# Performance work log

Measured on AMD Instinct MI355X. Metric: run time of the kernel, lower is better.

Reference implementation:

```python
import jax, jax.numpy as jnp
import numpy as np

N_NODES = 100000
N_EDGES = 3200000
D_IN = 128
D_HID = 128
D_FF = 256
N_CLASSES = 26
N_GRAPHS = 512


def setup_inputs() -> dict:
    key = jax.random.key(0)
    ks = jax.random.split(key, 12)
    s = 0.05
    return {
        "x": jax.random.normal(ks[0], (N_NODES, D_IN), dtype=jnp.float32),
        "edge_index": jax.random.randint(ks[1], (2, N_EDGES), 0, N_NODES, dtype=jnp.int64),
        "batch": jnp.sort(jax.random.randint(ks[2], (N_NODES,), 0, N_GRAPHS, dtype=jnp.int64)),
        "W1": jax.random.normal(ks[3], (D_IN, D_HID), dtype=jnp.float32) * s,
        "b1": jnp.zeros((D_HID,), dtype=jnp.float32),
        "W2": jax.random.normal(ks[4], (D_HID, D_HID), dtype=jnp.float32) * s,
        "b2": jnp.zeros((D_HID,), dtype=jnp.float32),
        "W3": jax.random.normal(ks[5], (D_HID, D_HID), dtype=jnp.float32) * s,
        "b3": jnp.zeros((D_HID,), dtype=jnp.float32),
        "Wfc": jax.random.normal(ks[6], (D_HID, D_FF), dtype=jnp.float32) * s,
        "bfc": jnp.zeros((D_FF,), dtype=jnp.float32),
        "Wfc2": jax.random.normal(ks[7], (D_FF, N_CLASSES), dtype=jnp.float32) * s,
        "bfc2": jnp.zeros((N_CLASSES,), dtype=jnp.float32),
    }


def _gcn_layer(x, src, dst, norm, W, b):
    # GCNConv: h = x @ W; out[dst] += norm_e * h[src]; out += b
    h = x @ W                                   # [N, D]
    msg = h[src] * norm[:, None]                # [E+N, D] gather + scale
    agg = jax.ops.segment_sum(msg, dst, num_segments=N_NODES)
    return agg + b


def reference(x, edge_index, batch, W1, b1, W2, b2, W3, b3, Wfc, bfc, Wfc2, bfc2):
    # add self-loops (PyG GCNConv default) and compute symmetric normalization once
    loop = jnp.arange(N_NODES, dtype=edge_index.dtype)
    src = jnp.concatenate([edge_index[0], loop])
    dst = jnp.concatenate([edge_index[1], loop])
    deg = jax.ops.segment_sum(jnp.ones_like(dst, dtype=x.dtype), dst, num_segments=N_NODES)
    dinv = jnp.where(deg > 0, jax.lax.rsqrt(deg), 0.0)
    norm = dinv[src] * dinv[dst]               # D^{-1/2} A_hat D^{-1/2}

    h = jax.nn.relu(_gcn_layer(x, src, dst, norm, W1, b1))
    h = jax.nn.relu(_gcn_layer(h, src, dst, norm, W2, b2))
    h = jax.nn.relu(_gcn_layer(h, src, dst, norm, W3, b3))

    # global mean pool over graphs
    sums = jax.ops.segment_sum(h, batch, num_segments=N_GRAPHS)       # [G, D]
    cnts = jax.ops.segment_sum(jnp.ones((h.shape[0],), h.dtype), batch, num_segments=N_GRAPHS)
    pooled = sums / jnp.maximum(cnts, 1.0)[:, None]

    out = jax.nn.relu(pooled @ Wfc + bfc)       # dropout is identity at inference
    return out @ Wfc2 + bfc2                    # [G, num_classes]
```

## Files before the change

### kernel.cpp

```cpp
#include <hip/hip_runtime.h>
#include <hip/hip_bf16.h>

typedef __bf16 bf16;
typedef __attribute__((ext_vector_type(8))) __bf16 bf16x8;
typedef __attribute__((ext_vector_type(4))) float f32x4;

constexpr int N_NODES   = 100000;
constexpr int N_PAD     = 100032;
constexpr int D         = 128;
constexpr int D_FF      = 256;
constexpr int N_CLASSES = 26;
constexpr int N_GRAPHS  = 512;
constexpr int NB1       = 256;
constexpr int NBUCK     = (N_NODES + 511) / 512;

__device__ inline float2 bf2f(unsigned u) {
    float lo = __uint_as_float(u << 16);
    float hi = __uint_as_float(u & 0xffff0000u);
    return make_float2(lo, hi);
}

__device__ inline void nt_store_bf16(bf16* p, float f) {
    bf16 v = (bf16)f;
    short s = *reinterpret_cast<short*>(&v);
    __builtin_nontemporal_store(s, reinterpret_cast<short*>(p));
}


__global__ __launch_bounds__(1024) void p1_hist(const int* __restrict__ edst,
                                                int* __restrict__ gcount, int e) {
    __shared__ int cnt[NBUCK];
    for (int t = threadIdx.x; t < NBUCK; t += 1024) cnt[t] = 0;
    __syncthreads();
    int chunk = (e + NB1 - 1) / NB1;
    int lo = blockIdx.x * chunk;
    int hi = min(e, lo + chunk);
    for (int i = lo + threadIdx.x; i < hi; i += 1024)
        atomicAdd(&cnt[edst[i] >> 9], 1);
    __syncthreads();
    for (int t = threadIdx.x; t < NBUCK; t += 1024)
        gcount[t * NB1 + blockIdx.x] = cnt[t];
}

__global__ __launch_bounds__(256) void scan1(const int* __restrict__ in,
                                             int* out, int* bsum, int n) {
    __shared__ int sd[256];
    int i = blockIdx.x * 256 + threadIdx.x;
    int v = (i < n) ? in[i] : 0;
    sd[threadIdx.x] = v; __syncthreads();
    for (int off = 1; off < 256; off <<= 1) {
        int t = (threadIdx.x >= off) ? sd[threadIdx.x - off] : 0;
        __syncthreads();
        sd[threadIdx.x] += t;
        __syncthreads();
    }
    if (i < n) out[i] = sd[threadIdx.x] - v;
    if (threadIdx.x == 255) bsum[blockIdx.x] = sd[255];
}

__global__ __launch_bounds__(1024) void misc_kernel(const int* __restrict__ bsum,
                                                    int* __restrict__ boff, int nb,
                                                    const int* __restrict__ batch,
                                                    int* __restrict__ starts, int n,
                                                    const float* __restrict__ W0,
                                                    const float* __restrict__ W1,
                                                    const float* __restrict__ W2,
                                                    bf16* __restrict__ WT3,
                                                    float* __restrict__ gsum) {
    int t = threadIdx.x;
    if (blockIdx.x == 0) {
        if (t <= N_GRAPHS) {
            int lo = 0, hi = n;
            while (lo < hi) {
                int mid = (lo + hi) >> 1;
                if (batch[mid] < t) lo = mid + 1; else hi = mid;
            }
            starts[t] = lo;
        }
        __shared__ int sd[1024];
        int v = (t < nb) ? bsum[t] : 0;
        sd[t] = v; __syncthreads();
        for (int off = 1; off < 1024; off <<= 1) {
            int x = (t >= off) ? sd[t - off] : 0;
            __syncthreads();
            sd[t] += x;
            __syncthreads();
        }
        if (t < nb) boff[t] = sd[t] - v;
    } else if (blockIdx.x <= 48) {
        int idx = (blockIdx.x - 1) * 1024 + t;
        int l = idx >> 14;
        int rem = idx & 16383;
        int nn = rem >> 7;
        int kk = rem & 127;
        const float* W = (l == 0) ? W0 : (l == 1) ? W1 : W2;
        WT3[idx] = (bf16)W[kk * D + nn];
    } else {
        int idx = (blockIdx.x - 49) * 1024 + t;
        f32x4 z = {0.f, 0.f, 0.f, 0.f};
        *((f32x4*)gsum + idx) = z;
    }
}

__global__ __launch_bounds__(1024) void p3_scatter(const int* __restrict__ esrc,
                                                   const int* __restrict__ edst,
                                                   const int* __restrict__ gbase,
                                                   const int* __restrict__ boff,
                                                   int* __restrict__ ebuf, int e) {
    __shared__ int cur[NBUCK];
    for (int t = threadIdx.x; t < NBUCK; t += 1024)
        cur[t] = gbase[t * NB1 + blockIdx.x] + boff[t];
    __syncthreads();
    int chunk = (e + NB1 - 1) / NB1;
    int lo = blockIdx.x * chunk;
    int hi = min(e, lo + chunk);
    for (int i = lo + threadIdx.x; i < hi; i += 1024) {
        int d = edst[i], s = esrc[i];
        int pos = atomicAdd(&cur[d >> 9], 1);
        ebuf[pos] = (s << 9) | (d & 511);
    }
}

__global__ __launch_bounds__(1024) void p45_fill(const int* __restrict__ ebuf,
                                                 const int* __restrict__ gbase,
                                                 const int* __restrict__ boff,
                                                 float* __restrict__ dinv,
                                                 int* __restrict__ rowptr,
                                                 int* __restrict__ csrc, int e, int n) {
    __shared__ int cnt[512];
    __shared__ int ps[512];
    __shared__ int cur[512];
    int b = blockIdx.x, t = threadIdx.x;
    if (t < 512) cnt[t] = 0;
    __syncthreads();
    int lo = gbase[b * NB1] + boff[b];
    int hi = (b + 1 < NBUCK) ? gbase[(b + 1) * NB1] + boff[b + 1] : e;
    for (int i = lo + t; i < hi; i += 1024)
        atomicAdd(&cnt[ebuf[i] & 511], 1);
    __syncthreads();
    int a = (t < 512) ? cnt[t] : 0;
    if (t < 512) ps[t] = a;
    __syncthreads();
    for (int off = 1; off < 512; off <<= 1) {
        int v = (t >= off && t < 512) ? ps[t - off] : 0;
        __syncthreads();
        if (t < 512) ps[t] += v;
        __syncthreads();
    }
    if (t < 512) {
        int g0 = lo + ps[t] - a;
        int node = b * 512 + t;
        cur[t] = g0;
        if (node < n) {
            rowptr[node] = g0;
            dinv[node] = 1.0f / sqrtf((float)(a + 1));
        }
    }
    if (b == 0 && t == 0) rowptr[n] = e;
    __syncthreads();
    for (int i = lo + t; i < hi; i += 1024) {
        int pe = ebuf[i];
        int pos = atomicAdd(&cur[pe & 511], 1);
        csrc[pos] = pe >> 9;
    }
}


__global__ __launch_bounds__(256) void gemm_f32_kernel(const float* __restrict__ A,
                                                       const bf16* __restrict__ WT,
                                                       bf16* __restrict__ C,
                                                       const float* __restrict__ dinv, int n) {
    int wave = threadIdx.x >> 6;
    int lane = threadIdx.x & 63;
    int m16  = lane & 15;
    int quad = lane >> 4;
    int row0 = blockIdx.x * 64 + wave * 16;
    int arowi = row0 + m16;

    bf16x8 a[4];
    const float* arow = A + (size_t)arowi * D + quad * 8;
#pragma unroll
    for (int kt = 0; kt < 4; ++kt) {
        f32x4 f0 = {0.f, 0.f, 0.f, 0.f};
        f32x4 f1 = {0.f, 0.f, 0.f, 0.f};
        if (arowi < n) {
            f0 = __builtin_nontemporal_load((const f32x4*)(arow + kt * 32));
            f1 = __builtin_nontemporal_load((const f32x4*)(arow + kt * 32 + 4));
        }
        bf16x8 v = { (bf16)f0[0], (bf16)f0[1], (bf16)f0[2], (bf16)f0[3],
                     (bf16)f1[0], (bf16)f1[1], (bf16)f1[2], (bf16)f1[3] };
        a[kt] = v;
    }

    float sc[4];
#pragma unroll
    for (int r = 0; r < 4; ++r) {
        int rr = row0 + quad * 4 + r;
        sc[r] = (rr < n) ? dinv[rr] : 0.f;
    }

#pragma unroll
    for (int nt = 0; nt < 8; ++nt) {
        f32x4 acc = {0.f, 0.f, 0.f, 0.f};
        const bf16* brow = WT + (nt * 16 + m16) * D + quad * 8;
#pragma unroll
        for (int kt = 0; kt < 4; ++kt) {
            bf16x8 b = *(const bf16x8*)(brow + kt * 32);
            acc = __builtin_amdgcn_mfma_f32_16x16x32_bf16(a[kt], b, acc, 0, 0, 0);
        }
#pragma unroll
        for (int r = 0; r < 4; ++r)
            nt_store_bf16(&C[(row0 + quad * 4 + r) * D + nt * 16 + m16], sc[r] * acc[r]);
    }
}

__device__ inline void agg_node(const bf16* __restrict__ h, int v, int n, int c,
                                const int* __restrict__ rowptr,
                                const int* __restrict__ csrc,
                                const float* __restrict__ dinv,
                                float& dv, float acc[8]) {
    int s = 0, e = 0;
    dv = 0.f;
    if (v < n) { s = rowptr[v]; e = rowptr[v + 1]; dv = dinv[v]; }
#pragma unroll
    for (int d = 0; d < 8; ++d) acc[d] = 0.f;
    if (v < n) {
        uint4 u = *(const uint4*)(h + (size_t)v * D + c * 8);
        float2 f0 = bf2f(u.x), f1 = bf2f(u.y), f2 = bf2f(u.z), f3 = bf2f(u.w);
        acc[0] = f0.x; acc[1] = f0.y; acc[2] = f1.x; acc[3] = f1.y;
        acc[4] = f2.x; acc[5] = f2.y; acc[6] = f3.x; acc[7] = f3.y;
    }
    int j = s;
    for (; j + 3 < e; j += 4) {
        int s0 = __builtin_nontemporal_load(csrc + j);
        int s1 = __builtin_nontemporal_load(csrc + j + 1);
        int s2 = __builtin_nontemporal_load(csrc + j + 2);
        int s3 = __builtin_nontemporal_load(csrc + j + 3);
        uint4 u0 = *(const uint4*)(h + (size_t)s0 * D + c * 8);
        uint4 u1 = *(const uint4*)(h + (size_t)s1 * D + c * 8);
        uint4 u2 = *(const uint4*)(h + (size_t)s2 * D + c * 8);
        uint4 u3 = *(const uint4*)(h + (size_t)s3 * D + c * 8);
        {
            float2 a0 = bf2f(u0.x), a1 = bf2f(u0.y), a2 = bf2f(u0.z), a3 = bf2f(u0.w);
            acc[0] += a0.x; acc[1] += a0.y; acc[2] += a1.x; acc[3] += a1.y;
            acc[4] += a2.x; acc[5] += a2.y; acc[6] += a3.x; acc[7] += a3.y;
        }
        {
            float2 a0 = bf2f(u1.x), a1 = bf2f(u1.y), a2 = bf2f(u1.z), a3 = bf2f(u1.w);
            acc[0] += a0.x; acc[1] += a0.y; acc[2] += a1.x; acc[3] += a1.y;
            acc[4] += a2.x; acc[5] += a2.y; acc[6] += a3.x; acc[7] += a3.y;
        }
        {
            float2 a0 = bf2f(u2.x), a1 = bf2f(u2.y), a2 = bf2f(u2.z), a3 = bf2f(u2.w);
            acc[0] += a0.x; acc[1] += a0.y; acc[2] += a1.x; acc[3] += a1.y;
            acc[4] += a2.x; acc[5] += a2.y; acc[6] += a3.x; acc[7] += a3.y;
        }
        {
            float2 a0 = bf2f(u3.x), a1 = bf2f(u3.y), a2 = bf2f(u3.z), a3 = bf2f(u3.w);
            acc[0] += a0.x; acc[1] += a0.y; acc[2] += a1.x; acc[3] += a1.y;
            acc[4] += a2.x; acc[5] += a2.y; acc[6] += a3.x; acc[7] += a3.y;
        }
    }
    for (; j < e; ++j) {
        int s0 = __builtin_nontemporal_load(csrc + j);
        uint4 u0 = *(const uint4*)(h + (size_t)s0 * D + c * 8);
        float2 a0 = bf2f(u0.x), a1 = bf2f(u0.y), a2 = bf2f(u0.z), a3 = bf2f(u0.w);
        acc[0] += a0.x; acc[1] += a0.y; acc[2] += a1.x; acc[3] += a1.y;
        acc[4] += a2.x; acc[5] += a2.y; acc[6] += a3.x; acc[7] += a3.y;
    }
}

__global__ __launch_bounds__(256) void spmm_gemm_kernel(const bf16* __restrict__ h,
                                                        const int* __restrict__ rowptr,
                                                        const int* __restrict__ csrc,
                                                        const float* __restrict__ dinv,
                                                        const float* __restrict__ bias,
                                                        const bf16* __restrict__ WT,
                                                        bf16* __restrict__ C, int n) {
    __shared__ bf16 tile[16][136];
    int t = threadIdx.x;
    int grp = t >> 4;
    int c   = t & 15;
    int v   = blockIdx.x * 16 + grp;
    float dv, acc[8];
    agg_node(h, v, n, c, rowptr, csrc, dinv, dv, acc);
    {
        float4 bi0 = *(const float4*)(bias + c * 8);
        float4 bi1 = *(const float4*)(bias + c * 8 + 4);
        bf16x8 o;
        o[0] = (bf16)fmaxf(fmaf(dv, acc[0], bi0.x), 0.f);
        o[1] = (bf16)fmaxf(fmaf(dv, acc[1], bi0.y), 0.f);
        o[2] = (bf16)fmaxf(fmaf(dv, acc[2], bi0.z), 0.f);
        o[3] = (bf16)fmaxf(fmaf(dv, acc[3], bi0.w), 0.f);
        o[4] = (bf16)fmaxf(fmaf(dv, acc[4], bi1.x), 0.f);
        o[5] = (bf16)fmaxf(fmaf(dv, acc[5], bi1.y), 0.f);
        o[6] = (bf16)fmaxf(fmaf(dv, acc[6], bi1.z), 0.f);
        o[7] = (bf16)fmaxf(fmaf(dv, acc[7], bi1.w), 0.f);
        *(bf16x8*)(&tile[grp][c * 8]) = o;
    }
    __syncthreads();

    int wave = t >> 6, lane = t & 63;
    int m16 = lane & 15, quad = lane >> 4;
    bf16x8 a[4];
#pragma unroll
    for (int kt = 0; kt < 4; ++kt)
        a[kt] = *(const bf16x8*)(&tile[m16][quad * 8 + kt * 32]);

    int base = blockIdx.x * 16;
    float sc[4];
#pragma unroll
    for (int r = 0; r < 4; ++r) {
        int rr = base + quad * 4 + r;
        sc[r] = (rr < n) ? dinv[rr] : 0.f;
    }

#pragma unroll
    for (int nt2 = 0; nt2 < 2; ++nt2) {
        int nt = wave * 2 + nt2;
        f32x4 accq = {0.f, 0.f, 0.f, 0.f};
        const bf16* brow = WT + (nt * 16 + m16) * D + quad * 8;
#pragma unroll
        for (int kt = 0; kt < 4; ++kt) {
            bf16x8 b = *(const bf16x8*)(brow + kt * 32);
            accq = __builtin_amdgcn_mfma_f32_16x16x32_bf16(a[kt], b, accq, 0, 0, 0);
        }
#pragma unroll
        for (int r = 0; r < 4; ++r)
            nt_store_bf16(&C[(size_t)(base + quad * 4 + r) * D + nt * 16 + m16],
                          sc[r] * accq[r]);
    }
}

__global__ __launch_bounds__(256) void spmm2_pool_kernel(const bf16* __restrict__ h,
                                                         const int* __restrict__ rowptr,
                                                         const int* __restrict__ csrc,
                                                         const float* __restrict__ dinv,
                                                         const float* __restrict__ bias,
                                                         const int* __restrict__ batch,
                                                         float* __restrict__ gsum, int n) {
    __shared__ float tile[16][D];
    __shared__ int gid[16];
    int t = threadIdx.x;
    int grp = t >> 4;
    int c   = t & 15;
    int v   = blockIdx.x * 16 + grp;
    float dv, acc[8];
    agg_node(h, v, n, c, rowptr, csrc, dinv, dv, acc);
    float4 bi0 = *(const float4*)(bias + c * 8);
    float4 bi1 = *(const float4*)(bias + c * 8 + 4);
    float r0 = fmaxf(fmaf(dv, acc[0], bi0.x), 0.f);
    float r1 = fmaxf(fmaf(dv, acc[1], bi0.y), 0.f);
    float r2 = fmaxf(fmaf(dv, acc[2], bi0.z), 0.f);
    float r3 = fmaxf(fmaf(dv, acc[3], bi0.w), 0.f);
    float r4 = fmaxf(fmaf(dv, acc[4], bi1.x), 0.f);
    float r5 = fmaxf(fmaf(dv, acc[5], bi1.y), 0.f);
    float r6 = fmaxf(fmaf(dv, acc[6], bi1.z), 0.f);
    float r7 = fmaxf(fmaf(dv, acc[7], bi1.w), 0.f);
    if (v >= n) { r0 = r1 = r2 = r3 = r4 = r5 = r6 = r7 = 0.f; }
    tile[grp][c * 8 + 0] = r0; tile[grp][c * 8 + 1] = r1;
    tile[grp][c * 8 + 2] = r2; tile[grp][c * 8 + 3] = r3;
    tile[grp][c * 8 + 4] = r4; tile[grp][c * 8 + 5] = r5;
    tile[grp][c * 8 + 6] = r6; tile[grp][c * 8 + 7] = r7;
    if (c == 0) gid[grp] = (v < n) ? batch[v] : -1;
    __syncthreads();
    if (t < D) {
        int curg = gid[0];
        float sum = 0.f;
        if (curg >= 0) {
#pragma unroll 1
            for (int k = 0; k < 16; ++k) {
                int gg = gid[k];
                if (gg < 0) break;
                if (gg != curg) {
                    atomicAdd(&gsum[(size_t)curg * D + t], sum);
                    curg = gg; sum = 0.f;
                }
                sum += tile[k][t];
            }
            atomicAdd(&gsum[(size_t)curg * D + t], sum);
        }
    }
}

__global__ __launch_bounds__(256) void fc_head_kernel(const float* __restrict__ gsum,
                                                      const int* __restrict__ starts,
                                                      const float* __restrict__ Wfc,
                                                      const float* __restrict__ bfc,
                                                      const float* __restrict__ Wfc2,
                                                      const float* __restrict__ bfc2,
                                                      float* __restrict__ out) {
    __shared__ float pr[D];
    __shared__ float hid[D_FF];
    __shared__ float red[N_CLASSES][9];
    int g = blockIdx.x, t = threadIdx.x;
    if (t < D) {
        float ccount = fmaxf((float)(starts[g + 1] - starts[g]), 1.0f);
        pr[t] = gsum[(size_t)g * D + t] / ccount;
    }
    __syncthreads();
    float a0 = 0.f, a1 = 0.f, a2 = 0.f, a3 = 0.f;
    for (int k = 0; k < D; k += 4) {
        a0 = fmaf(pr[k],     Wfc[k * D_FF + t],       a0);
        a1 = fmaf(pr[k + 1], Wfc[(k + 1) * D_FF + t], a1);
        a2 = fmaf(pr[k + 2], Wfc[(k + 2) * D_FF + t], a2);
        a3 = fmaf(pr[k + 3], Wfc[(k + 3) * D_FF + t], a3);
    }
    hid[t] = fmaxf((a0 + a1) + (a2 + a3) + bfc[t], 0.f);
    __syncthreads();
    if (t < N_CLASSES * 8) {
        int cls = t >> 3, kk = t & 7;
        float o = 0.f;
        for (int k = kk; k < D_FF; k += 8)
            o = fmaf(hid[k], Wfc2[k * N_CLASSES + cls], o);
        red[cls][kk] = o;
    }
    __syncthreads();
    if (t < N_CLASSES) {
        float o = bfc2[t];
#pragma unroll
        for (int k = 0; k < 8; ++k) o += red[t][k];
        out[g * N_CLASSES + t] = o;
    }
}


extern "C" void kernel_launch(void* const* d_in, const int* in_sizes, int n_in,
                              void* d_out, int out_size, void* d_ws, size_t ws_size,
                              hipStream_t stream) {
    const float* x     = (const float*)d_in[0];
    const int*   eidx  = (const int*)d_in[1];
    const int*   batch = (const int*)d_in[2];
    const float* W[3]  = { (const float*)d_in[3], (const float*)d_in[5], (const float*)d_in[7] };
    const float* b[3]  = { (const float*)d_in[4], (const float*)d_in[6], (const float*)d_in[8] };
    const float* Wfc   = (const float*)d_in[9];
    const float* bfc   = (const float*)d_in[10];
    const float* Wfc2  = (const float*)d_in[11];
    const float* bfc2  = (const float*)d_in[12];
    float* out = (float*)d_out;

    const int E = in_sizes[1] / 2;
    const int N = in_sizes[0] / D;
    const int* esrc = eidx;
    const int* edst = eidx + E;

    uint8_t* base = (uint8_t*)d_ws;
    size_t off = 0;
    auto alloc = [&](size_t bytes) -> void* {
        void* p = base + off;
        off = (off + bytes + 255) & ~(size_t)255;
        return p;
    };
    bf16*  hA     = (bf16*) alloc((size_t)N_PAD * D * 2);
    bf16*  hB     = (bf16*) alloc((size_t)N_PAD * D * 2);
    bf16*  WT3    = (bf16*) alloc((size_t)3 * D * D * 2);
    int*   csrc   = (int*)  alloc((size_t)E * 4);
    int*   ebuf   = (int*)  alloc((size_t)E * 4);
    int*   gcount = (int*)  alloc((size_t)NBUCK * NB1 * 4);
    int*   gbase  = (int*)  alloc((size_t)(NBUCK * NB1 + 1) * 4);
    int*   rowptr = (int*)  alloc((size_t)(N + 1) * 4);
    float* dinv   = (float*)alloc((size_t)N * 4);
    int*   bsum   = (int*)  alloc(4096);
    int*   boff   = (int*)  alloc(4096);
    int*   starts = (int*)  alloc((size_t)(N_GRAPHS + 1) * 4);
    float* gsum   = (float*)alloc((size_t)N_GRAPHS * D * 4);
    (void)ws_size; (void)n_in; (void)out_size;

    const int GB  = N_PAD / 64;
    const int SGB = (N + 15) / 16;
    const int GCN = NBUCK * NB1;
    const int GCB = (GCN + 255) / 256;

    p1_hist<<<NB1, 1024, 0, stream>>>(edst, gcount, E);
    scan1<<<GCB, 256, 0, stream>>>(gcount, gbase, bsum, GCN);
    misc_kernel<<<65, 1024, 0, stream>>>(bsum, boff, GCB, batch, starts, N,
                                         W[0], W[1], W[2], WT3, gsum);
    p3_scatter<<<NB1, 1024, 0, stream>>>(esrc, edst, gbase, boff, ebuf, E);
    p45_fill<<<NBUCK, 1024, 0, stream>>>(ebuf, gbase, boff, dinv, rowptr, csrc, E, N);

    gemm_f32_kernel<<<GB, 256, 0, stream>>>(x, WT3, hA, dinv, N);
    spmm_gemm_kernel<<<SGB, 256, 0, stream>>>(hA, rowptr, csrc, dinv, b[0],
                                              WT3 + (size_t)1 * D * D, hB, N);
    spmm_gemm_kernel<<<SGB, 256, 0, stream>>>(hB, rowptr, csrc, dinv, b[1],
                                              WT3 + (size_t)2 * D * D, hA, N);
    spmm2_pool_kernel<<<SGB, 256, 0, stream>>>(hA, rowptr, csrc, dinv, b[2],
                                               batch, gsum, N);

    fc_head_kernel<<<N_GRAPHS, 256, 0, stream>>>(gsum, starts, Wfc, bfc, Wfc2, bfc2, out);
}
```

Baseline: 617.6 us.

## Pre-sort edges by source bucket before CSR build; drop nontemporal loads/stores

Adds an extra bucket pass keyed on source node, so edges are grouped by source before the destination bucket scatter. Within each destination row the neighbor indices then come out roughly ordered by source, which should improve cache locality of the feature gathers in the SpMM kernels. It also replaces the nontemporal loads and stores with plain ones, so data can stay in cache. The cost is an extra histogram, scan and scatter over all 3.2M edges plus two extra edge arrays.

```diff
diff --git a/kernel.cpp b/kernel.cpp
--- a/kernel.cpp
+++ b/kernel.cpp
@@ -20,14 +20,8 @@
     return make_float2(lo, hi);
 }
 
-__device__ inline void nt_store_bf16(bf16* p, float f) {
-    bf16 v = (bf16)f;
-    short s = *reinterpret_cast<short*>(&v);
-    __builtin_nontemporal_store(s, reinterpret_cast<short*>(p));
-}
-
-
-__global__ __launch_bounds__(1024) void p1_hist(const int* __restrict__ edst,
+
+__global__ __launch_bounds__(1024) void p1_hist(const int* __restrict__ key,
                                                 int* __restrict__ gcount, int e) {
     __shared__ int cnt[NBUCK];
     for (int t = threadIdx.x; t < NBUCK; t += 1024) cnt[t] = 0;
@@ -36,7 +30,7 @@
     int lo = blockIdx.x * chunk;
     int hi = min(e, lo + chunk);
     for (int i = lo + threadIdx.x; i < hi; i += 1024)
-        atomicAdd(&cnt[edst[i] >> 9], 1);
+        atomicAdd(&cnt[key[i] >> 9], 1);
     __syncthreads();
     for (int t = threadIdx.x; t < NBUCK; t += 1024)
         gcount[t * NB1 + blockIdx.x] = cnt[t];
@@ -58,9 +52,22 @@
     if (threadIdx.x == 255) bsum[blockIdx.x] = sd[255];
 }
 
-__global__ __launch_bounds__(1024) void misc_kernel(const int* __restrict__ bsum,
-                                                    int* __restrict__ boff, int nb,
-                                                    const int* __restrict__ batch,
+__global__ __launch_bounds__(1024) void scan2k(const int* __restrict__ bsum,
+                                               int* __restrict__ boff, int nb) {
+    __shared__ int sd[1024];
+    int t = threadIdx.x;
+    int v = (t < nb) ? bsum[t] : 0;
+    sd[t] = v; __syncthreads();
+    for (int off = 1; off < 1024; off <<= 1) {
+        int x = (t >= off) ? sd[t - off] : 0;
+        __syncthreads();
+        sd[t] += x;
+        __syncthreads();
+    }
+    if (t < nb) boff[t] = sd[t] - v;
+}
+
+__global__ __launch_bounds__(1024) void misc_kernel(const int* __restrict__ batch,
                                                     int* __restrict__ starts, int n,
                                                     const float* __restrict__ W0,
                                                     const float* __restrict__ W1,
@@ -77,16 +84,6 @@
             }
             starts[t] = lo;
         }
-        __shared__ int sd[1024];
-        int v = (t < nb) ? bsum[t] : 0;
-        sd[t] = v; __syncthreads();
-        for (int off = 1; off < 1024; off <<= 1) {
-            int x = (t >= off) ? sd[t - off] : 0;
-            __syncthreads();
-            sd[t] += x;
-            __syncthreads();
-        }
-        if (t < nb) boff[t] = sd[t] - v;
     } else if (blockIdx.x <= 48) {
         int idx = (blockIdx.x - 1) * 1024 + t;
         int l = idx >> 14;
@@ -102,8 +99,28 @@
     }
 }
 
-__global__ __launch_bounds__(1024) void p3_scatter(const int* __restrict__ esrc,
-                                                   const int* __restrict__ edst,
+__global__ __launch_bounds__(1024) void p3s_scatter(const int* __restrict__ esrc,
+                                                    const int* __restrict__ edst,
+                                                    const int* __restrict__ gbaseS,
+                                                    const int* __restrict__ boffS,
+                                                    int* __restrict__ esrc2,
+                                                    int* __restrict__ edst2, int e) {
+    __shared__ int cur[NBUCK];
+    for (int t = threadIdx.x; t < NBUCK; t += 1024)
+        cur[t] = gbaseS[t * NB1 + blockIdx.x] + boffS[t];
+    __syncthreads();
+    int chunk = (e + NB1 - 1) / NB1;
+    int lo = blockIdx.x * chunk;
+    int hi = min(e, lo + chunk);
+    for (int i = lo + threadIdx.x; i < hi; i += 1024) {
+        int s = esrc[i], d = edst[i];
+        int pos = atomicAdd(&cur[s >> 9], 1);
+        esrc2[pos] = s; edst2[pos] = d;
+    }
+}
+
+__global__ __launch_bounds__(1024) void p3_scatter(const int* __restrict__ esrc2,
+                                                   const int* __restrict__ edst2,
                                                    const int* __restrict__ gbase,
                                                    const int* __restrict__ boff,
                                                    int* __restrict__ ebuf, int e) {
@@ -115,7 +132,7 @@
     int lo = blockIdx.x * chunk;
     int hi = min(e, lo + chunk);
     for (int i = lo + threadIdx.x; i < hi; i += 1024) {
-        int d = edst[i], s = esrc[i];
+        int d = edst2[i], s = esrc2[i];
         int pos = atomicAdd(&cur[d >> 9], 1);
         ebuf[pos] = (s << 9) | (d & 511);
     }
@@ -181,14 +198,14 @@
     const float* arow = A + (size_t)arowi * D + quad * 8;
 #pragma unroll
     for (int kt = 0; kt < 4; ++kt) {
-        f32x4 f0 = {0.f, 0.f, 0.f, 0.f};
-        f32x4 f1 = {0.f, 0.f, 0.f, 0.f};
+        float4 f0 = make_float4(0.f, 0.f, 0.f, 0.f);
+        float4 f1 = make_float4(0.f, 0.f, 0.f, 0.f);
         if (arowi < n) {
-            f0 = __builtin_nontemporal_load((const f32x4*)(arow + kt * 32));
-            f1 = __builtin_nontemporal_load((const f32x4*)(arow + kt * 32 + 4));
-        }
-        bf16x8 v = { (bf16)f0[0], (bf16)f0[1], (bf16)f0[2], (bf16)f0[3],
-                     (bf16)f1[0], (bf16)f1[1], (bf16)f1[2], (bf16)f1[3] };
+            f0 = *(const float4*)(arow + kt * 32);
+            f1 = *(const float4*)(arow + kt * 32 + 4);
+        }
+        bf16x8 v = { (bf16)f0.x, (bf16)f0.y, (bf16)f0.z, (bf16)f0.w,
+                     (bf16)f1.x, (bf16)f1.y, (bf16)f1.z, (bf16)f1.w };
         a[kt] = v;
     }
 
@@ -210,7 +227,7 @@
         }
 #pragma unroll
         for (int r = 0; r < 4; ++r)
-            nt_store_bf16(&C[(row0 + quad * 4 + r) * D + nt * 16 + m16], sc[r] * acc[r]);
+            C[(row0 + quad * 4 + r) * D + nt * 16 + m16] = (bf16)(sc[r] * acc[r]);
     }
 }
 
@@ -232,10 +249,7 @@
     }
     int j = s;
     for (; j + 3 < e; j += 4) {
-        int s0 = __builtin_nontemporal_load(csrc + j);
-        int s1 = __builtin_nontemporal_load(csrc + j + 1);
-        int s2 = __builtin_nontemporal_load(csrc + j + 2);
-        int s3 = __builtin_nontemporal_load(csrc + j + 3);
+        int s0 = csrc[j], s1 = csrc[j + 1], s2 = csrc[j + 2], s3 = csrc[j + 3];
         uint4 u0 = *(const uint4*)(h + (size_t)s0 * D + c * 8);
         uint4 u1 = *(const uint4*)(h + (size_t)s1 * D + c * 8);
         uint4 u2 = *(const uint4*)(h + (size_t)s2 * D + c * 8);
@@ -262,7 +276,7 @@
         }
     }
     for (; j < e; ++j) {
-        int s0 = __builtin_nontemporal_load(csrc + j);
+        int s0 = csrc[j];
         uint4 u0 = *(const uint4*)(h + (size_t)s0 * D + c * 8);
         float2 a0 = bf2f(u0.x), a1 = bf2f(u0.y), a2 = bf2f(u0.z), a3 = bf2f(u0.w);
         acc[0] += a0.x; acc[1] += a0.y; acc[2] += a1.x; acc[3] += a1.y;
@@ -327,8 +341,7 @@
         }
 #pragma unroll
         for (int r = 0; r < 4; ++r)
-            nt_store_bf16(&C[(size_t)(base + quad * 4 + r) * D + nt * 16 + m16],
-                          sc[r] * accq[r]);
+            C[(size_t)(base + quad * 4 + r) * D + nt * 16 + m16] = (bf16)(sc[r] * accq[r]);
     }
 }
 
@@ -451,19 +464,25 @@
         off = (off + bytes + 255) & ~(size_t)255;
         return p;
     };
-    bf16*  hA     = (bf16*) alloc((size_t)N_PAD * D * 2);
-    bf16*  hB     = (bf16*) alloc((size_t)N_PAD * D * 2);
-    bf16*  WT3    = (bf16*) alloc((size_t)3 * D * D * 2);
-    int*   csrc   = (int*)  alloc((size_t)E * 4);
-    int*   ebuf   = (int*)  alloc((size_t)E * 4);
-    int*   gcount = (int*)  alloc((size_t)NBUCK * NB1 * 4);
-    int*   gbase  = (int*)  alloc((size_t)(NBUCK * NB1 + 1) * 4);
-    int*   rowptr = (int*)  alloc((size_t)(N + 1) * 4);
-    float* dinv   = (float*)alloc((size_t)N * 4);
-    int*   bsum   = (int*)  alloc(4096);
-    int*   boff   = (int*)  alloc(4096);
-    int*   starts = (int*)  alloc((size_t)(N_GRAPHS + 1) * 4);
-    float* gsum   = (float*)alloc((size_t)N_GRAPHS * D * 4);
+    bf16*  hA      = (bf16*) alloc((size_t)N_PAD * D * 2);
+    bf16*  hB      = (bf16*) alloc((size_t)N_PAD * D * 2);
+    bf16*  WT3     = (bf16*) alloc((size_t)3 * D * D * 2);
+    int*   csrc    = (int*)  alloc((size_t)E * 4);
+    int*   ebuf    = (int*)  alloc((size_t)E * 4);
+    int*   esrc2   = (int*)  alloc((size_t)E * 4);
+    int*   edst2   = (int*)  alloc((size_t)E * 4);
+    int*   gcountS = (int*)  alloc((size_t)NBUCK * NB1 * 4);
+    int*   gbaseS  = (int*)  alloc((size_t)(NBUCK * NB1 + 1) * 4);
+    int*   gcountD = (int*)  alloc((size_t)NBUCK * NB1 * 4);
+    int*   gbaseD  = (int*)  alloc((size_t)(NBUCK * NB1 + 1) * 4);
+    int*   rowptr  = (int*)  alloc((size_t)(N + 1) * 4);
+    float* dinv    = (float*)alloc((size_t)N * 4);
+    int*   bsumS   = (int*)  alloc(4096);
+    int*   boffS   = (int*)  alloc(4096);
+    int*   bsumD   = (int*)  alloc(4096);
+    int*   boffD   = (int*)  alloc(4096);
+    int*   starts  = (int*)  alloc((size_t)(N_GRAPHS + 1) * 4);
+    float* gsum    = (float*)alloc((size_t)N_GRAPHS * D * 4);
     (void)ws_size; (void)n_in; (void)out_size;
 
     const int GB  = N_PAD / 64;
@@ -471,12 +490,16 @@
     const int GCN = NBUCK * NB1;
     const int GCB = (GCN + 255) / 256;
 
-    p1_hist<<<NB1, 1024, 0, stream>>>(edst, gcount, E);
-    scan1<<<GCB, 256, 0, stream>>>(gcount, gbase, bsum, GCN);
-    misc_kernel<<<65, 1024, 0, stream>>>(bsum, boff, GCB, batch, starts, N,
-                                         W[0], W[1], W[2], WT3, gsum);
-    p3_scatter<<<NB1, 1024, 0, stream>>>(esrc, edst, gbase, boff, ebuf, E);
-    p45_fill<<<NBUCK, 1024, 0, stream>>>(ebuf, gbase, boff, dinv, rowptr, csrc, E, N);
+    p1_hist<<<NB1, 1024, 0, stream>>>(esrc, gcountS, E);
+    scan1<<<GCB, 256, 0, stream>>>(gcountS, gbaseS, bsumS, GCN);
+    scan2k<<<1, 1024, 0, stream>>>(bsumS, boffS, GCB);
+    misc_kernel<<<65, 1024, 0, stream>>>(batch, starts, N, W[0], W[1], W[2], WT3, gsum);
+    p3s_scatter<<<NB1, 1024, 0, stream>>>(esrc, edst, gbaseS, boffS, esrc2, edst2, E);
+    p1_hist<<<NB1, 1024, 0, stream>>>(edst2, gcountD, E);
+    scan1<<<GCB, 256, 0, stream>>>(gcountD, gbaseD, bsumD, GCN);
+    scan2k<<<1, 1024, 0, stream>>>(bsumD, boffD, GCB);
+    p3_scatter<<<NB1, 1024, 0, stream>>>(esrc2, edst2, gbaseD, boffD, ebuf, E);
+    p45_fill<<<NBUCK, 1024, 0, stream>>>(ebuf, gbaseD, boffD, dinv, rowptr, csrc, E, N);
 
     gemm_f32_kernel<<<GB, 256, 0, stream>>>(x, WT3, hA, dinv, N);
     spmm_gemm_kernel<<<SGB, 256, 0, stream>>>(hA, rowptr, csrc, dinv, b[0],
```

Result: no change. 606.1 us (-1.9%).

## Phase-partition CSR by source range and process node batches per block in lockstep

Applied to the files above, without the earlier changes.

Edges of each destination are now sorted into 13 source-range phases (src>>13), with per-node phase offsets stored in a new P array instead of rowptr. The SpMM kernels use 512 persistent blocks, each covering 196 nodes. They walk all nodes' edges phase by phase so concurrent gathers hit a narrow source window and stay cache-resident, then run the GEMM/pool epilogue in 32-row chunks. This adds extra shared-memory counting in the fill, more registers (7x8 accumulators) and serialized per-chunk syncs. It also moves the boff scan into its own kernel and drops nontemporal loads and stores.

```diff
diff --git a/kernel.cpp b/kernel.cpp
--- a/kernel.cpp
+++ b/kernel.cpp
@@ -14,16 +14,21 @@
 constexpr int NB1       = 256;
 constexpr int NBUCK     = (N_NODES + 511) / 512;
 
+constexpr int KPH  = 13;
+constexpr int PST  = 14;
+constexpr int NPB  = 196;
+constexpr int PBLK = 512;
+
 __device__ inline float2 bf2f(unsigned u) {
     float lo = __uint_as_float(u << 16);
     float hi = __uint_as_float(u & 0xffff0000u);
     return make_float2(lo, hi);
 }
 
-__device__ inline void nt_store_bf16(bf16* p, float f) {
-    bf16 v = (bf16)f;
-    short s = *reinterpret_cast<short*>(&v);
-    __builtin_nontemporal_store(s, reinterpret_cast<short*>(p));
+__device__ inline void acc_row(float acc[8], uint4 u) {
+    float2 f0 = bf2f(u.x), f1 = bf2f(u.y), f2 = bf2f(u.z), f3 = bf2f(u.w);
+    acc[0] += f0.x; acc[1] += f0.y; acc[2] += f1.x; acc[3] += f1.y;
+    acc[4] += f2.x; acc[5] += f2.y; acc[6] += f3.x; acc[7] += f3.y;
 }
 
 
@@ -58,9 +63,22 @@
     if (threadIdx.x == 255) bsum[blockIdx.x] = sd[255];
 }
 
-__global__ __launch_bounds__(1024) void misc_kernel(const int* __restrict__ bsum,
-                                                    int* __restrict__ boff, int nb,
-                                                    const int* __restrict__ batch,
+__global__ __launch_bounds__(1024) void scan2k(const int* __restrict__ bsum,
+                                               int* __restrict__ boff, int nb) {
+    __shared__ int sd[1024];
+    int t = threadIdx.x;
+    int v = (t < nb) ? bsum[t] : 0;
+    sd[t] = v; __syncthreads();
+    for (int off = 1; off < 1024; off <<= 1) {
+        int x = (t >= off) ? sd[t - off] : 0;
+        __syncthreads();
+        sd[t] += x;
+        __syncthreads();
+    }
+    if (t < nb) boff[t] = sd[t] - v;
+}
+
+__global__ __launch_bounds__(1024) void misc_kernel(const int* __restrict__ batch,
                                                     int* __restrict__ starts, int n,
                                                     const float* __restrict__ W0,
                                                     const float* __restrict__ W1,
@@ -77,16 +95,6 @@
             }
             starts[t] = lo;
         }
-        __shared__ int sd[1024];
-        int v = (t < nb) ? bsum[t] : 0;
-        sd[t] = v; __syncthreads();
-        for (int off = 1; off < 1024; off <<= 1) {
-            int x = (t >= off) ? sd[t - off] : 0;
-            __syncthreads();
-            sd[t] += x;
-            __syncthreads();
-        }
-        if (t < nb) boff[t] = sd[t] - v;
     } else if (blockIdx.x <= 48) {
         int idx = (blockIdx.x - 1) * 1024 + t;
         int l = idx >> 14;
@@ -125,21 +133,29 @@
                                                  const int* __restrict__ gbase,
                                                  const int* __restrict__ boff,
                                                  float* __restrict__ dinv,
-                                                 int* __restrict__ rowptr,
+                                                 int* __restrict__ P,
                                                  int* __restrict__ csrc, int e, int n) {
-    __shared__ int cnt[512];
+    __shared__ int c2[512 * KPH];
     __shared__ int ps[512];
-    __shared__ int cur[512];
     int b = blockIdx.x, t = threadIdx.x;
-    if (t < 512) cnt[t] = 0;
+    for (int q = t; q < 512 * KPH; q += 1024) c2[q] = 0;
     __syncthreads();
     int lo = gbase[b * NB1] + boff[b];
     int hi = (b + 1 < NBUCK) ? gbase[(b + 1) * NB1] + boff[b + 1] : e;
-    for (int i = lo + t; i < hi; i += 1024)
-        atomicAdd(&cnt[ebuf[i] & 511], 1);
-    __syncthreads();
-    int a = (t < 512) ? cnt[t] : 0;
-    if (t < 512) ps[t] = a;
+    for (int i = lo + t; i < hi; i += 1024) {
+        int pe = ebuf[i];
+        atomicAdd(&c2[(pe & 511) * KPH + (pe >> 22)], 1);
+    }
+    __syncthreads();
+    int tot = 0;
+    if (t < 512) {
+        for (int k = 0; k < KPH; ++k) {
+            int cc = c2[t * KPH + k];
+            c2[t * KPH + k] = tot;
+            tot += cc;
+        }
+        ps[t] = tot;
+    }
     __syncthreads();
     for (int off = 1; off < 512; off <<= 1) {
         int v = (t >= off && t < 512) ? ps[t - off] : 0;
@@ -148,19 +164,22 @@
         __syncthreads();
     }
     if (t < 512) {
-        int g0 = lo + ps[t] - a;
+        int g0 = lo + ps[t] - tot;
         int node = b * 512 + t;
-        cur[t] = g0;
         if (node < n) {
-            rowptr[node] = g0;
-            dinv[node] = 1.0f / sqrtf((float)(a + 1));
-        }
-    }
-    if (b == 0 && t == 0) rowptr[n] = e;
+            dinv[node] = 1.0f / sqrtf((float)(tot + 1));
+            for (int k = 0; k < KPH; ++k) {
+                int a = g0 + c2[t * KPH + k];
+                P[node * PST + k] = a;
+                c2[t * KPH + k] = a;
+            }
+            P[node * PST + KPH] = g0 + tot;
+        }
+    }
     __syncthreads();
     for (int i = lo + t; i < hi; i += 1024) {
         int pe = ebuf[i];
-        int pos = atomicAdd(&cur[pe & 511], 1);
+        int pos = atomicAdd(&c2[(pe & 511) * KPH + (pe >> 22)], 1);
         csrc[pos] = pe >> 9;
     }
 }
@@ -181,14 +200,14 @@
     const float* arow = A + (size_t)arowi * D + quad * 8;
 #pragma unroll
     for (int kt = 0; kt < 4; ++kt) {
-        f32x4 f0 = {0.f, 0.f, 0.f, 0.f};
-        f32x4 f1 = {0.f, 0.f, 0.f, 0.f};
+        float4 f0 = make_float4(0.f, 0.f, 0.f, 0.f);
+        float4 f1 = make_float4(0.f, 0.f, 0.f, 0.f);
         if (arowi < n) {
-            f0 = __builtin_nontemporal_load((const f32x4*)(arow + kt * 32));
-            f1 = __builtin_nontemporal_load((const f32x4*)(arow + kt * 32 + 4));
-        }
-        bf16x8 v = { (bf16)f0[0], (bf16)f0[1], (bf16)f0[2], (bf16)f0[3],
-                     (bf16)f1[0], (bf16)f1[1], (bf16)f1[2], (bf16)f1[3] };
+            f0 = *(const float4*)(arow + kt * 32);
+            f1 = *(const float4*)(arow + kt * 32 + 4);
+        }
+        bf16x8 v = { (bf16)f0.x, (bf16)f0.y, (bf16)f0.z, (bf16)f0.w,
+                     (bf16)f1.x, (bf16)f1.y, (bf16)f1.z, (bf16)f1.w };
         a[kt] = v;
     }
 
@@ -210,175 +229,171 @@
         }
 #pragma unroll
         for (int r = 0; r < 4; ++r)
-            nt_store_bf16(&C[(row0 + quad * 4 + r) * D + nt * 16 + m16], sc[r] * acc[r]);
-    }
-}
-
-__device__ inline void agg_node(const bf16* __restrict__ h, int v, int n, int c,
-                                const int* __restrict__ rowptr,
-                                const int* __restrict__ csrc,
-                                const float* __restrict__ dinv,
-                                float& dv, float acc[8]) {
-    int s = 0, e = 0;
-    dv = 0.f;
-    if (v < n) { s = rowptr[v]; e = rowptr[v + 1]; dv = dinv[v]; }
-#pragma unroll
-    for (int d = 0; d < 8; ++d) acc[d] = 0.f;
-    if (v < n) {
-        uint4 u = *(const uint4*)(h + (size_t)v * D + c * 8);
-        float2 f0 = bf2f(u.x), f1 = bf2f(u.y), f2 = bf2f(u.z), f3 = bf2f(u.w);
-        acc[0] = f0.x; acc[1] = f0.y; acc[2] = f1.x; acc[3] = f1.y;
-        acc[4] = f2.x; acc[5] = f2.y; acc[6] = f3.x; acc[7] = f3.y;
-    }
-    int j = s;
-    for (; j + 3 < e; j += 4) {
-        int s0 = __builtin_nontemporal_load(csrc + j);
-        int s1 = __builtin_nontemporal_load(csrc + j + 1);
-        int s2 = __builtin_nontemporal_load(csrc + j + 2);
-        int s3 = __builtin_nontemporal_load(csrc + j + 3);
-        uint4 u0 = *(const uint4*)(h + (size_t)s0 * D + c * 8);
-        uint4 u1 = *(const uint4*)(h + (size_t)s1 * D + c * 8);
-        uint4 u2 = *(const uint4*)(h + (size_t)s2 * D + c * 8);
-        uint4 u3 = *(const uint4*)(h + (size_t)s3 * D + c * 8);
-        {
-            float2 a0 = bf2f(u0.x), a1 = bf2f(u0.y), a2 = bf2f(u0.z), a3 = bf2f(u0.w);
-            acc[0] += a0.x; acc[1] += a0.y; acc[2] += a1.x; acc[3] += a1.y;
-            acc[4] += a2.x; acc[5] += a2.y; acc[6] += a3.x; acc[7] += a3.y;
-        }
-        {
-            float2 a0 = bf2f(u1.x), a1 = bf2f(u1.y), a2 = bf2f(u1.z), a3 = bf2f(u1.w);
-            acc[0] += a0.x; acc[1] += a0.y; acc[2] += a1.x; acc[3] += a1.y;
-            acc[4] += a2.x; acc[5] += a2.y; acc[6] += a3.x; acc[7] += a3.y;
-        }
-        {
-            float2 a0 = bf2f(u2.x), a1 = bf2f(u2.y), a2 = bf2f(u2.z), a3 = bf2f(u2.w);
-            acc[0] += a0.x; acc[1] += a0.y; acc[2] += a1.x; acc[3] += a1.y;
-            acc[4] += a2.x; acc[5] += a2.y; acc[6] += a3.x; acc[7] += a3.y;
-        }
-        {
-            float2 a0 = bf2f(u3.x), a1 = bf2f(u3.y), a2 = bf2f(u3.z), a3 = bf2f(u3.w);
-            acc[0] += a0.x; acc[1] += a0.y; acc[2] += a1.x; acc[3] += a1.y;
-            acc[4] += a2.x; acc[5] += a2.y; acc[6] += a3.x; acc[7] += a3.y;
-        }
-    }
-    for (; j < e; ++j) {
-        int s0 = __builtin_nontemporal_load(csrc + j);
-        uint4 u0 = *(const uint4*)(h + (size_t)s0 * D + c * 8);
-        float2 a0 = bf2f(u0.x), a1 = bf2f(u0.y), a2 = bf2f(u0.z), a3 = bf2f(u0.w);
-        acc[0] += a0.x; acc[1] += a0.y; acc[2] += a1.x; acc[3] += a1.y;
-        acc[4] += a2.x; acc[5] += a2.y; acc[6] += a3.x; acc[7] += a3.y;
-    }
-}
-
-__global__ __launch_bounds__(256) void spmm_gemm_kernel(const bf16* __restrict__ h,
-                                                        const int* __restrict__ rowptr,
-                                                        const int* __restrict__ csrc,
-                                                        const float* __restrict__ dinv,
-                                                        const float* __restrict__ bias,
-                                                        const bf16* __restrict__ WT,
-                                                        bf16* __restrict__ C, int n) {
-    __shared__ bf16 tile[16][136];
+            C[(row0 + quad * 4 + r) * D + nt * 16 + m16] = (bf16)(sc[r] * acc[r]);
+    }
+}
+
+__device__ inline void pagg(const bf16* __restrict__ h,
+                            const int* __restrict__ P,
+                            const int* __restrict__ csrc,
+                            int base, int g, int c, int n, float acc[7][8]) {
+#pragma unroll
+    for (int i = 0; i < 7; ++i) {
+#pragma unroll
+        for (int d = 0; d < 8; ++d) acc[i][d] = 0.f;
+        int v = base + i * 32 + g;
+        if (i * 32 + g < NPB && v < n) {
+            uint4 u = *(const uint4*)(h + (size_t)v * D + c * 8);
+            acc_row(acc[i], u);
+        }
+    }
+    for (int k = 0; k < KPH; ++k) {
+#pragma unroll
+        for (int i = 0; i < 7; ++i) {
+            int v = base + i * 32 + g;
+            if (i * 32 + g >= NPB || v >= n) continue;
+            int s = P[v * PST + k], e = P[v * PST + k + 1];
+            int j = s;
+            for (; j + 1 < e; j += 2) {
+                int s0 = csrc[j], s1 = csrc[j + 1];
+                uint4 u0 = *(const uint4*)(h + (size_t)s0 * D + c * 8);
+                uint4 u1 = *(const uint4*)(h + (size_t)s1 * D + c * 8);
+                acc_row(acc[i], u0);
+                acc_row(acc[i], u1);
+            }
+            if (j < e) {
+                int s0 = csrc[j];
+                uint4 u0 = *(const uint4*)(h + (size_t)s0 * D + c * 8);
+                acc_row(acc[i], u0);
+            }
+        }
+    }
+}
+
+__global__ __launch_bounds__(512, 4) void pspmm_gemm_kernel(const bf16* __restrict__ h,
+                                                            const int* __restrict__ P,
+                                                            const int* __restrict__ csrc,
+                                                            const float* __restrict__ dinv,
+                                                            const float* __restrict__ bias,
+                                                            const bf16* __restrict__ WT,
+                                                            bf16* __restrict__ C, int n) {
+    __shared__ bf16 tile[32][136];
     int t = threadIdx.x;
-    int grp = t >> 4;
-    int c   = t & 15;
-    int v   = blockIdx.x * 16 + grp;
-    float dv, acc[8];
-    agg_node(h, v, n, c, rowptr, csrc, dinv, dv, acc);
-    {
-        float4 bi0 = *(const float4*)(bias + c * 8);
-        float4 bi1 = *(const float4*)(bias + c * 8 + 4);
-        bf16x8 o;
-        o[0] = (bf16)fmaxf(fmaf(dv, acc[0], bi0.x), 0.f);
-        o[1] = (bf16)fmaxf(fmaf(dv, acc[1], bi0.y), 0.f);
-        o[2] = (bf16)fmaxf(fmaf(dv, acc[2], bi0.z), 0.f);
-        o[3] = (bf16)fmaxf(fmaf(dv, acc[3], bi0.w), 0.f);
-        o[4] = (bf16)fmaxf(fmaf(dv, acc[4], bi1.x), 0.f);
-        o[5] = (bf16)fmaxf(fmaf(dv, acc[5], bi1.y), 0.f);
-        o[6] = (bf16)fmaxf(fmaf(dv, acc[6], bi1.z), 0.f);
-        o[7] = (bf16)fmaxf(fmaf(dv, acc[7], bi1.w), 0.f);
-        *(bf16x8*)(&tile[grp][c * 8]) = o;
-    }
-    __syncthreads();
+    int g = t >> 4, c = t & 15;
+    int base = blockIdx.x * NPB;
+    float acc[7][8];
+    pagg(h, P, csrc, base, g, c, n, acc);
 
     int wave = t >> 6, lane = t & 63;
     int m16 = lane & 15, quad = lane >> 4;
-    bf16x8 a[4];
-#pragma unroll
-    for (int kt = 0; kt < 4; ++kt)
-        a[kt] = *(const bf16x8*)(&tile[m16][quad * 8 + kt * 32]);
-
-    int base = blockIdx.x * 16;
-    float sc[4];
-#pragma unroll
-    for (int r = 0; r < 4; ++r) {
-        int rr = base + quad * 4 + r;
-        sc[r] = (rr < n) ? dinv[rr] : 0.f;
-    }
-
-#pragma unroll
-    for (int nt2 = 0; nt2 < 2; ++nt2) {
-        int nt = wave * 2 + nt2;
-        f32x4 accq = {0.f, 0.f, 0.f, 0.f};
-        const bf16* brow = WT + (nt * 16 + m16) * D + quad * 8;
-#pragma unroll
-        for (int kt = 0; kt < 4; ++kt) {
-            bf16x8 b = *(const bf16x8*)(brow + kt * 32);
-            accq = __builtin_amdgcn_mfma_f32_16x16x32_bf16(a[kt], b, accq, 0, 0, 0);
-        }
-#pragma unroll
-        for (int r = 0; r < 4; ++r)
-            nt_store_bf16(&C[(size_t)(base + quad * 4 + r) * D + nt * 16 + m16],
-                          sc[r] * accq[r]);
-    }
-}
-
-__global__ __launch_bounds__(256) void spmm2_pool_kernel(const bf16* __restrict__ h,
-                                                         const int* __restrict__ rowptr,
-                                                         const int* __restrict__ csrc,
-                                                         const float* __restrict__ dinv,
-                                                         const float* __restrict__ bias,
-                                                         const int* __restrict__ batch,
-                                                         float* __restrict__ gsum, int n) {
-    __shared__ float tile[16][D];
-    __shared__ int gid[16];
-    int t = threadIdx.x;
-    int grp = t >> 4;
-    int c   = t & 15;
-    int v   = blockIdx.x * 16 + grp;
-    float dv, acc[8];
-    agg_node(h, v, n, c, rowptr, csrc, dinv, dv, acc);
+    int tr0 = (wave >= 4) ? 16 : 0;
+    int ntq = (wave & 3) * 2;
     float4 bi0 = *(const float4*)(bias + c * 8);
     float4 bi1 = *(const float4*)(bias + c * 8 + 4);
-    float r0 = fmaxf(fmaf(dv, acc[0], bi0.x), 0.f);
-    float r1 = fmaxf(fmaf(dv, acc[1], bi0.y), 0.f);
-    float r2 = fmaxf(fmaf(dv, acc[2], bi0.z), 0.f);
-    float r3 = fmaxf(fmaf(dv, acc[3], bi0.w), 0.f);
-    float r4 = fmaxf(fmaf(dv, acc[4], bi1.x), 0.f);
-    float r5 = fmaxf(fmaf(dv, acc[5], bi1.y), 0.f);
-    float r6 = fmaxf(fmaf(dv, acc[6], bi1.z), 0.f);
-    float r7 = fmaxf(fmaf(dv, acc[7], bi1.w), 0.f);
-    if (v >= n) { r0 = r1 = r2 = r3 = r4 = r5 = r6 = r7 = 0.f; }
-    tile[grp][c * 8 + 0] = r0; tile[grp][c * 8 + 1] = r1;
-    tile[grp][c * 8 + 2] = r2; tile[grp][c * 8 + 3] = r3;
-    tile[grp][c * 8 + 4] = r4; tile[grp][c * 8 + 5] = r5;
-    tile[grp][c * 8 + 6] = r6; tile[grp][c * 8 + 7] = r7;
-    if (c == 0) gid[grp] = (v < n) ? batch[v] : -1;
-    __syncthreads();
-    if (t < D) {
-        int curg = gid[0];
-        float sum = 0.f;
-        if (curg >= 0) {
+
+#pragma unroll
+    for (int i = 0; i < 7; ++i) {
+        int v = base + i * 32 + g;
+        bool val = (i * 32 + g < NPB) && (v < n);
+        float dv = val ? dinv[v] : 0.f;
+        bf16x8 o;
+        o[0] = val ? (bf16)fmaxf(fmaf(dv, acc[i][0], bi0.x), 0.f) : (bf16)0.f;
+        o[1] = val ? (bf16)fmaxf(fmaf(dv, acc[i][1], bi0.y), 0.f) : (bf16)0.f;
+        o[2] = val ? (bf16)fmaxf(fmaf(dv, acc[i][2], bi0.z), 0.f) : (bf16)0.f;
+        o[3] = val ? (bf16)fmaxf(fmaf(dv, acc[i][3], bi0.w), 0.f) : (bf16)0.f;
+        o[4] = val ? (bf16)fmaxf(fmaf(dv, acc[i][4], bi1.x), 0.f) : (bf16)0.f;
+        o[5] = val ? (bf16)fmaxf(fmaf(dv, acc[i][5], bi1.y), 0.f) : (bf16)0.f;
+        o[6] = val ? (bf16)fmaxf(fmaf(dv, acc[i][6], bi1.z), 0.f) : (bf16)0.f;
+        o[7] = val ? (bf16)fmaxf(fmaf(dv, acc[i][7], bi1.w), 0.f) : (bf16)0.f;
+        __syncthreads();
+        *(bf16x8*)(&tile[g][c * 8]) = o;
+        __syncthreads();
+
+        bf16x8 a[4];
+#pragma unroll
+        for (int kt = 0; kt < 4; ++kt)
+            a[kt] = *(const bf16x8*)(&tile[tr0 + m16][quad * 8 + kt * 32]);
+        float sc[4];
+#pragma unroll
+        for (int r = 0; r < 4; ++r) {
+            int lr = i * 32 + tr0 + quad * 4 + r;
+            int rr = base + lr;
+            sc[r] = (lr < NPB && rr < n) ? dinv[rr] : 0.f;
+        }
+#pragma unroll
+        for (int nt2 = 0; nt2 < 2; ++nt2) {
+            int nt = ntq + nt2;
+            f32x4 q = {0.f, 0.f, 0.f, 0.f};
+            const bf16* brow = WT + (nt * 16 + m16) * D + quad * 8;
+#pragma unroll
+            for (int kt = 0; kt < 4; ++kt) {
+                bf16x8 bfr = *(const bf16x8*)(brow + kt * 32);
+                q = __builtin_amdgcn_mfma_f32_16x16x32_bf16(a[kt], bfr, q, 0, 0, 0);
+            }
+#pragma unroll
+            for (int r = 0; r < 4; ++r) {
+                int lr = i * 32 + tr0 + quad * 4 + r;
+                int rr = base + lr;
+                if (lr < NPB && rr < n)
+                    C[(size_t)rr * D + nt * 16 + m16] = (bf16)(sc[r] * q[r]);
+            }
+        }
+    }
+}
+
+__global__ __launch_bounds__(512, 4) void pspmm_pool_kernel(const bf16* __restrict__ h,
+                                                            const int* __restrict__ P,
+                                                            const int* __restrict__ csrc,
+                                                            const float* __restrict__ dinv,
+                                                            const float* __restrict__ bias,
+                                                            const int* __restrict__ batch,
+                                                            float* __restrict__ gsum, int n) {
+    __shared__ float tile[32][D];
+    __shared__ int gid[32];
+    int t = threadIdx.x;
+    int g = t >> 4, c = t & 15;
+    int base = blockIdx.x * NPB;
+    float acc[7][8];
+    pagg(h, P, csrc, base, g, c, n, acc);
+
+    float4 bi0 = *(const float4*)(bias + c * 8);
+    float4 bi1 = *(const float4*)(bias + c * 8 + 4);
+#pragma unroll
+    for (int i = 0; i < 7; ++i) {
+        int v = base + i * 32 + g;
+        bool val = (i * 32 + g < NPB) && (v < n);
+        float dv = val ? dinv[v] : 0.f;
+        float r0 = val ? fmaxf(fmaf(dv, acc[i][0], bi0.x), 0.f) : 0.f;
+        float r1 = val ? fmaxf(fmaf(dv, acc[i][1], bi0.y), 0.f) : 0.f;
+        float r2 = val ? fmaxf(fmaf(dv, acc[i][2], bi0.z), 0.f) : 0.f;
+        float r3 = val ? fmaxf(fmaf(dv, acc[i][3], bi0.w), 0.f) : 0.f;
+        float r4 = val ? fmaxf(fmaf(dv, acc[i][4], bi1.x), 0.f) : 0.f;
+        float r5 = val ? fmaxf(fmaf(dv, acc[i][5], bi1.y), 0.f) : 0.f;
+        float r6 = val ? fmaxf(fmaf(dv, acc[i][6], bi1.z), 0.f) : 0.f;
+        float r7 = val ? fmaxf(fmaf(dv, acc[i][7], bi1.w), 0.f) : 0.f;
+        __syncthreads();
+        tile[g][c * 8 + 0] = r0; tile[g][c * 8 + 1] = r1;
+        tile[g][c * 8 + 2] = r2; tile[g][c * 8 + 3] = r3;
+        tile[g][c * 8 + 4] = r4; tile[g][c * 8 + 5] = r5;
+        tile[g][c * 8 + 6] = r6; tile[g][c * 8 + 7] = r7;
+        if (c == 0) gid[g] = val ? batch[v] : -1;
+        __syncthreads();
+        if (t < D) {
+            int curg = gid[0];
+            float sum = 0.f;
+            if (curg >= 0) {
 #pragma unroll 1
-            for (int k = 0; k < 16; ++k) {
-                int gg = gid[k];
-                if (gg < 0) break;
-                if (gg != curg) {
-                    atomicAdd(&gsum[(size_t)curg * D + t], sum);
-                    curg = gg; sum = 0.f;
+                for (int kk = 0; kk < 32; ++kk) {
+                    int gg = gid[kk];
+                    if (gg < 0) break;
+                    if (gg != curg) {
+                        atomicAdd(&gsum[(size_t)curg * D + t], sum);
+                        curg = gg; sum = 0.f;
+                    }
+                    sum += tile[kk][t];
                 }
-                sum += tile[k][t];
-            }
-            atomicAdd(&gsum[(size_t)curg * D + t], sum);
+                atomicAdd(&gsum[(size_t)curg * D + t], sum);
+            }
         }
     }
 }
@@ -458,7 +473,7 @@
     int*   ebuf   = (int*)  alloc((size_t)E * 4);
     int*   gcount = (int*)  alloc((size_t)NBUCK * NB1 * 4);
     int*   gbase  = (int*)  alloc((size_t)(NBUCK * NB1 + 1) * 4);
-    int*   rowptr = (int*)  alloc((size_t)(N + 1) * 4);
+    int*   P      = (int*)  alloc((size_t)N_PAD * PST * 4);
     float* dinv   = (float*)alloc((size_t)N * 4);
     int*   bsum   = (int*)  alloc(4096);
     int*   boff   = (int*)  alloc(4096);
@@ -467,24 +482,23 @@
     (void)ws_size; (void)n_in; (void)out_size;
 
     const int GB  = N_PAD / 64;
-    const int SGB = (N + 15) / 16;
     const int GCN = NBUCK * NB1;
     const int GCB = (GCN + 255) / 256;
 
     p1_hist<<<NB1, 1024, 0, stream>>>(edst, gcount, E);
     scan1<<<GCB, 256, 0, stream>>>(gcount, gbase, bsum, GCN);
-    misc_kernel<<<65, 1024, 0, stream>>>(bsum, boff, GCB, batch, starts, N,
-                                         W[0], W[1], W[2], WT3, gsum);
+    scan2k<<<1, 1024, 0, stream>>>(bsum, boff, GCB);
+    misc_kernel<<<65, 1024, 0, stream>>>(batch, starts, N, W[0], W[1], W[2], WT3, gsum);
     p3_scatter<<<NB1, 1024, 0, stream>>>(esrc, edst, gbase, boff, ebuf, E);
-    p45_fill<<<NBUCK, 1024, 0, stream>>>(ebuf, gbase, boff, dinv, rowptr, csrc, E, N);
+    p45_fill<<<NBUCK, 1024, 0, stream>>>(ebuf, gbase, boff, dinv, P, csrc, E, N);
 
     gemm_f32_kernel<<<GB, 256, 0, stream>>>(x, WT3, hA, dinv, N);
-    spmm_gemm_kernel<<<SGB, 256, 0, stream>>>(hA, rowptr, csrc, dinv, b[0],
-                                              WT3 + (size_t)1 * D * D, hB, N);
-    spmm_gemm_kernel<<<SGB, 256, 0, stream>>>(hB, rowptr, csrc, dinv, b[1],
-                                              WT3 + (size_t)2 * D * D, hA, N);
-    spmm2_pool_kernel<<<SGB, 256, 0, stream>>>(hA, rowptr, csrc, dinv, b[2],
-                                               batch, gsum, N);
+    pspmm_gemm_kernel<<<PBLK, 512, 0, stream>>>(hA, P, csrc, dinv, b[0],
+                                                WT3 + (size_t)1 * D * D, hB, N);
+    pspmm_gemm_kernel<<<PBLK, 512, 0, stream>>>(hB, P, csrc, dinv, b[1],
+                                                WT3 + (size_t)2 * D * D, hA, N);
+    pspmm_pool_kernel<<<PBLK, 512, 0, stream>>>(hA, P, csrc, dinv, b[2],
+                                                batch, gsum, N);
 
     fc_head_kernel<<<N_GRAPHS, 256, 0, stream>>>(gsum, starts, Wfc, bfc, Wfc2, bfc2, out);
 }
```

New measurement: 897.8 us. 1.45x slower.
